# Kernel optimization log

Hardware: AMD Instinct MI355X
Metric: run time of the kernel (lower is better)

## Reference

```python
import jax, jax.numpy as jnp
import numpy as np

NUM_HEADS = 12
TOPK = 90


def setup_inputs() -> dict:
    key = jax.random.key(0)
    k1, k2, k3 = jax.random.split(key, 3)
    B, N, C = 8, 512, 768
    x = jax.random.normal(k1, (B, N, C), dtype=jnp.float32)
    qkv_w = jax.random.normal(k2, (3 * C, C), dtype=jnp.float32) * (C ** -0.5)
    proj_w = jax.random.normal(k3, (C, C), dtype=jnp.float32) * (C ** -0.5)
    proj_b = jnp.zeros((C,), dtype=jnp.float32)
    return {"x": x, "qkv_w": qkv_w, "proj_w": proj_w, "proj_b": proj_b, "islast": 0}


def reference(x, qkv_w, proj_w, proj_b, islast):
    B, N, C = x.shape
    H = NUM_HEADS
    hd = C // H
    scale = hd ** -0.5
    # qkv projection (no bias), split into q,k,v heads: [B,H,N,hd]
    qkv = (x @ qkv_w.T).reshape(B, N, 3, H, hd).transpose(2, 0, 3, 1, 4)
    q, k, v = qkv[0], qkv[1], qkv[2]
    attn = jnp.einsum('bhnd,bhmd->bhnm', q, k) * scale  # [B,H,N,N]
    if not islast:
        # keep only the top-k scores per row (kth-value threshold == topk mask)
        kth = jax.lax.top_k(attn, TOPK)[0][..., -1:]  # [B,H,N,1]
        attn = jnp.where(attn >= kth, attn, -jnp.inf)
    attn = jax.nn.softmax(attn, axis=-1)
    out = jnp.einsum('bhnm,bhmd->bnhd', attn, v).reshape(B, N, C)
    out = out @ proj_w.T + proj_b
    return out, attn
```

## Files before the change

kernel.cpp:

```cpp
#include <hip/hip_runtime.h>
#include <math.h>

#define BB 8
#define NN 512
#define CC 768
#define HH 12
#define HD 64
#define TOPK 90
#define QKV_ELEMS (BB*HH*NN*HD)
#define KC 2304

typedef __attribute__((ext_vector_type(8))) short short8;
typedef __attribute__((ext_vector_type(4))) float floatx4;

__device__ inline unsigned short f2bf(float f) {
    unsigned int u = __float_as_uint(f);
    u += 0x7FFFu + ((u >> 16) & 1u);
    return (unsigned short)(u >> 16);
}
__device__ inline float bf2f(unsigned short h) {
    return __uint_as_float(((unsigned int)h) << 16);
}

template<bool IS_A>
__global__ __launch_bounds__(256) void split_k(const float* __restrict__ in,
                                               unsigned short* __restrict__ o2,
                                               int total) {
    int idx = blockIdx.x * 256 + threadIdx.x;
    if (idx >= total) return;
    int e = idx * 4;
    int m = e / CC, kk = e - m * CC;
    float4 f = *(const float4*)(in + e);
    ushort4 hi, lo;
    hi.x = f2bf(f.x); lo.x = f2bf(f.x - bf2f(hi.x));
    hi.y = f2bf(f.y); lo.y = f2bf(f.y - bf2f(hi.y));
    hi.z = f2bf(f.z); lo.z = f2bf(f.z - bf2f(hi.z));
    hi.w = f2bf(f.w); lo.w = f2bf(f.w - bf2f(hi.w));
    unsigned short* base = o2 + (size_t)m * KC + kk;
    *(ushort4*)(base)        = hi;
    *(ushort4*)(base + CC)   = IS_A ? hi : lo;
    *(ushort4*)(base + 2*CC) = IS_A ? lo : hi;
}

template<int NCOLS, bool QKV_EPI>
__global__ __launch_bounds__(256) void gemm_split(const unsigned short* __restrict__ A,
                                                  const unsigned short* __restrict__ Bm,
                                                  const float* __restrict__ bias,
                                                  float* __restrict__ out,
                                                  unsigned short* __restrict__ qh,
                                                  unsigned short* __restrict__ ql,
                                                  unsigned short* __restrict__ kh,
                                                  unsigned short* __restrict__ kl,
                                                  unsigned short* __restrict__ vth,
                                                  unsigned short* __restrict__ vtl) {
    __shared__ char lds[32768];
    const int bm = blockIdx.x, bn = blockIdx.y;
    const int tid  = threadIdx.x;
    const int wave = tid >> 6, lane = tid & 63;
    const int wm = wave >> 1, wn = wave & 1;
    const int quad = lane >> 4, r = lane & 15;

    const unsigned short* gbase[8];
#pragma unroll
    for (int i = 0; i < 8; ++i) {
        int c = tid + i*256;
        int s = c & 1023;
        int m = s >> 3, octp = s & 7, oct = octp ^ (m & 7);
        gbase[i] = (i < 4 ? A  + (size_t)(bm*128 + m) * KC
                          : Bm + (size_t)(bn*128 + m) * KC) + oct*8;
    }

    int aoff[2][4], boff[2][4];
#pragma unroll
    for (int kb = 0; kb < 2; ++kb)
#pragma unroll
        for (int i = 0; i < 4; ++i) {
            int ra = wm*64 + i*16 + r;
            int rb2 = wn*64 + i*16 + r;
            aoff[kb][i] = (ra*8 + ((kb*4 + quad) ^ (ra & 7))) * 16;
            boff[kb][i] = 16384 + (rb2*8 + ((kb*4 + quad) ^ (rb2 & 7))) * 16;
        }

    floatx4 acc[4][4];
#pragma unroll
    for (int i = 0; i < 4; ++i)
#pragma unroll
        for (int j = 0; j < 4; ++j)
            acc[i][j] = (floatx4){0.f, 0.f, 0.f, 0.f};

    for (int it = 0; it < KC/64; ++it) {
        __syncthreads();
#pragma unroll
        for (int i = 0; i < 8; ++i) {
            __builtin_amdgcn_global_load_lds(
                (const __attribute__((address_space(1))) unsigned int*)gbase[i],
                (__attribute__((address_space(3))) unsigned int*)(lds + i*4096 + wave*1024),
                16, 0, 0);
            gbase[i] += 64;
        }
        asm volatile("s_waitcnt vmcnt(0)" ::: "memory");
        __syncthreads();

#pragma unroll
        for (int kb = 0; kb < 2; ++kb) {
            short8 af[4], bf[4];
#pragma unroll
            for (int i = 0; i < 4; ++i) af[i] = *(const short8*)(lds + aoff[kb][i]);
#pragma unroll
            for (int j = 0; j < 4; ++j) bf[j] = *(const short8*)(lds + boff[kb][j]);
#pragma unroll
            for (int i = 0; i < 4; ++i)
#pragma unroll
                for (int j = 0; j < 4; ++j)
                    acc[i][j] = __builtin_amdgcn_mfma_f32_16x16x32_bf16(af[i], bf[j], acc[i][j], 0, 0, 0);
        }
    }

    if (QKV_EPI) {
#pragma unroll
        for (int j = 0; j < 4; ++j) {
            int col = bn*128 + wn*64 + j*16 + r;
            int t = col / CC;
            int rem = col - t*CC;
            int h = rem >> 6, d = rem & 63;
            if (t == 2) {
#pragma unroll
                for (int i = 0; i < 4; ++i) {
                    int m0 = bm*128 + wm*64 + i*16 + quad*4;
                    int b = m0 >> 9, n0 = m0 & 511;
                    ushort4 hi, lo;
                    hi.x = f2bf(acc[i][j][0]); lo.x = f2bf(acc[i][j][0] - bf2f(hi.x));
                    hi.y = f2bf(acc[i][j][1]); lo.y = f2bf(acc[i][j][1] - bf2f(hi.y));
                    hi.z = f2bf(acc[i][j][2]); lo.z = f2bf(acc[i][j][2] - bf2f(hi.z));
                    hi.w = f2bf(acc[i][j][3]); lo.w = f2bf(acc[i][j][3] - bf2f(hi.w));
                    size_t off = ((size_t)((b*HH + h)*HD + d))*NN + n0;
                    *(ushort4*)(vth + off) = hi;
                    *(ushort4*)(vtl + off) = lo;
                }
            } else {
                unsigned short* ph = (t == 0) ? qh : kh;
                unsigned short* pl = (t == 0) ? ql : kl;
#pragma unroll
                for (int i = 0; i < 4; ++i) {
#pragma unroll
                    for (int e = 0; e < 4; ++e) {
                        int m = bm*128 + wm*64 + i*16 + quad*4 + e;
                        int b = m >> 9, nrow = m & 511;
                        size_t idx = ((size_t)(b*HH + h)*NN + nrow)*HD + d;
                        float val = acc[i][j][e];
                        unsigned short hi = f2bf(val);
                        ph[idx] = hi;
                        pl[idx] = f2bf(val - bf2f(hi));
                    }
                }
            }
        }
    } else {
#pragma unroll
        for (int j = 0; j < 4; ++j) {
            int col = bn*128 + wn*64 + j*16 + r;
            float bv = bias[col];
#pragma unroll
            for (int i = 0; i < 4; ++i) {
#pragma unroll
                for (int e = 0; e < 4; ++e) {
                    int m = bm*128 + wm*64 + i*16 + quad*4 + e;
                    out[(size_t)m*NCOLS + col] = acc[i][j][e] + bv;
                }
            }
        }
    }
}

__global__ __launch_bounds__(256, 1) void attn_scores_k(
        const unsigned short* __restrict__ qh, const unsigned short* __restrict__ ql,
        const unsigned short* __restrict__ kh, const unsigned short* __restrict__ kl,
        const unsigned short* __restrict__ vth, const unsigned short* __restrict__ vtl,
        const int* __restrict__ islast, float* __restrict__ attn,
        unsigned short* __restrict__ Ao) {

    __shared__ char smem[34816];
    unsigned short* qs = (unsigned short*)smem;
    char* ks = smem + 18432;

    const int bh = blockIdx.x % 96;
    const int rb = blockIdx.x / 96;
    const int tid = threadIdx.x;
    const int wv = tid >> 6, lane = tid & 63;
    const int quad = lane >> 4, r = lane & 15;
    const int b = bh / HH, h = bh % HH;

    const unsigned short* gq[2] = { qh + ((size_t)bh*NN + rb*64)*HD,
                                    ql + ((size_t)bh*NN + rb*64)*HD };
#pragma unroll
    for (int i = 0; i < 4; ++i) {
        int s = tid + i*256;
        int hl = s >> 9, s2 = s & 511;
        int row = s2 >> 3, oct = s2 & 7;
        short8 val = *(const short8*)(gq[hl] + row*HD + oct*8);
        *(short8*)&qs[(hl*64 + row)*72 + oct*8] = val;
    }
    __syncthreads();

    short8 afr[6];
    {
        const int arow = wv*16 + r;
#pragma unroll
        for (int t = 0; t < 3; ++t) {
            int src = (t == 2) ? 1 : 0;
#pragma unroll
            for (int half = 0; half < 2; ++half)
                afr[t*2+half] = *(const short8*)&qs[(src*64 + arow)*72 + half*32 + quad*8];
        }
    }

    floatx4 acc[32];
#pragma unroll
    for (int ct = 0; ct < 32; ++ct) acc[ct] = (floatx4){0.f,0.f,0.f,0.f};

    const unsigned short* gk[2] = { kh + (size_t)bh*NN*HD, kl + (size_t)bh*NN*HD };

    for (int ch = 0; ch < 8; ++ch) {
        __syncthreads();
#pragma unroll
        for (int i = 0; i < 4; ++i) {
            int s = tid + i*256;
            int hl = s >> 9, s2 = s & 511;
            int row = s2 >> 3, octp = s2 & 7;
            int oct = octp ^ (row & 7);
            const unsigned short* src = gk[hl] + (size_t)(ch*64 + row)*HD + oct*8;
            __builtin_amdgcn_global_load_lds(
                (const __attribute__((address_space(1))) unsigned int*)src,
                (__attribute__((address_space(3))) unsigned int*)(ks + (size_t)(i*256 + wv*64)*16),
                16, 0, 0);
        }
        asm volatile("s_waitcnt vmcnt(0)" ::: "memory");
        __syncthreads();

#pragma unroll
        for (int ctl = 0; ctl < 4; ++ctl) {
            const int ct = ch*4 + ctl;
            const int n = ctl*16 + r;
#pragma unroll
            for (int t = 0; t < 3; ++t) {
                const int srcB = (t == 1) ? 1 : 0;
#pragma unroll
                for (int half = 0; half < 2; ++half) {
                    const int oct = (half*4 + quad) ^ (n & 7);
                    short8 bfr = *(const short8*)(ks + srcB*8192 + n*128 + oct*16);
                    acc[ct] = __builtin_amdgcn_mfma_f32_16x16x32_bf16(afr[t*2+half], bfr, acc[ct], 0, 0, 0);
                }
            }
        }
    }

    const int lastv = islast[0];

#pragma unroll
    for (int e = 0; e < 4; ++e) {
        unsigned int key[32];
#pragma unroll
        for (int ct = 0; ct < 32; ++ct) {
            unsigned int t = __float_as_uint(acc[ct][e] * 0.125f);
            key[ct] = (t & 0x80000000u) ? ~t : (t | 0x80000000u);
        }

        unsigned int kth = 0u;
        if (!lastv) {
            unsigned int uo = key[0], ua = key[0];
#pragma unroll
            for (int ct = 1; ct < 32; ++ct) { uo |= key[ct]; ua &= key[ct]; }
#pragma unroll
            for (int off = 1; off <= 8; off <<= 1) {
                uo |= __shfl_xor(uo, off);
                ua &= __shfl_xor(ua, off);
            }
            unsigned int diff = uo ^ ua;
            int bit = 31 - __clz(diff);
            unsigned int am = 0xFFFFFFFFu;
            int kk = TOPK, cntA = 512;
            int done = (diff == 0u);
            while (__ballot(!done) != 0ull) {
                if (!done) {
                    unsigned int m1 = 0u;
#pragma unroll
                    for (int ct = 0; ct < 32; ++ct)
                        m1 |= ((key[ct] >> bit) & 1u) << ct;
                    int c1 = __popc(am & m1);
                    c1 += __shfl_xor(c1, 1);
                    c1 += __shfl_xor(c1, 2);
                    c1 += __shfl_xor(c1, 4);
                    c1 += __shfl_xor(c1, 8);
                    if (kk <= c1) { am &= m1; cntA = c1; }
                    else          { kk -= c1; am &= ~m1; cntA -= c1; }
                    --bit;
                    done = (cntA == kk) | (kk == 1) | (bit < 0);
                }
            }
            unsigned int mn = 0xFFFFFFFFu, mx = 0u;
#pragma unroll
            for (int ct = 0; ct < 32; ++ct) {
                if ((am >> ct) & 1u) {
                    mn = mn < key[ct] ? mn : key[ct];
                    mx = mx > key[ct] ? mx : key[ct];
                }
            }
#pragma unroll
            for (int off = 1; off <= 8; off <<= 1) {
                unsigned int mns = __shfl_xor(mn, off), mxs = __shfl_xor(mx, off);
                mn = mn < mns ? mn : mns; mx = mx > mxs ? mx : mxs;
            }
            kth = (kk == 1) ? mx : mn;
        }

        unsigned int umx = key[0];
#pragma unroll
        for (int ct = 1; ct < 32; ++ct) umx = umx > key[ct] ? umx : key[ct];
#pragma unroll
        for (int off = 1; off <= 8; off <<= 1) {
            unsigned int t2 = __shfl_xor(umx, off);
            umx = umx > t2 ? umx : t2;
        }
        float fmx = __uint_as_float((umx & 0x80000000u) ? (umx & 0x7FFFFFFFu) : ~umx);
        float sum = 0.f;
#pragma unroll
        for (int ct = 0; ct < 32; ++ct) {
            unsigned int uu = key[ct];
            float f = __uint_as_float((uu & 0x80000000u) ? (uu & 0x7FFFFFFFu) : ~uu);
            float ev = (lastv || uu >= kth) ? __expf(f - fmx) : 0.f;
            acc[ct][e] = ev;
            sum += ev;
        }
#pragma unroll
        for (int off = 1; off <= 8; off <<= 1) sum += __shfl_xor(sum, off);
        const float inv = 1.f / sum;
        float* arow = attn + ((size_t)bh*NN + rb*64 + wv*16 + quad*4 + e) * NN;
#pragma unroll
        for (int ct = 0; ct < 32; ++ct) {
            float p = acc[ct][e] * inv;
            acc[ct][e] = p;
            arow[ct*16 + r] = p;
        }
    }

    unsigned short* pls = (unsigned short*)smem;
    char* vhs = smem + 10240;
    char* vls = smem + 18432;
    const unsigned short* gvh = vth + (size_t)bh*HD*NN;
    const unsigned short* gvl = vtl + (size_t)bh*HD*NN;

    floatx4 accO[4];
#pragma unroll
    for (int j = 0; j < 4; ++j) accO[j] = (floatx4){0.f,0.f,0.f,0.f};

    for (int ch = 0; ch < 8; ++ch) {
        __syncthreads();
#pragma unroll
        for (int ctl = 0; ctl < 4; ++ctl) {
            int col = ctl*16 + r;
#pragma unroll
            for (int e = 0; e < 4; ++e)
                pls[(wv*16 + quad*4 + e)*80 + col] = f2bf(acc[ch*4 + ctl][e]);
        }
#pragma unroll
        for (int i = 0; i < 2; ++i) {
            int s = tid + i*256;
            int d = s >> 3, octp = s & 7, oct = octp ^ (d & 7);
            size_t goff = (size_t)d*NN + ch*64 + oct*8;
            __builtin_amdgcn_global_load_lds(
                (const __attribute__((address_space(1))) unsigned int*)(gvh + goff),
                (__attribute__((address_space(3))) unsigned int*)(vhs + (i*256 + wv*64)*16),
                16, 0, 0);
            __builtin_amdgcn_global_load_lds(
                (const __attribute__((address_space(1))) unsigned int*)(gvl + goff),
                (__attribute__((address_space(3))) unsigned int*)(vls + (i*256 + wv*64)*16),
                16, 0, 0);
        }
        asm volatile("s_waitcnt vmcnt(0)" ::: "memory");
        __syncthreads();

#pragma unroll
        for (int kb = 0; kb < 2; ++kb) {
            short8 af = *(const short8*)&pls[(wv*16 + r)*80 + kb*32 + quad*8];
#pragma unroll
            for (int j = 0; j < 4; ++j) {
                int d = j*16 + r;
                int oct = (kb*4 + quad) ^ (d & 7);
                short8 bh8 = *(const short8*)(vhs + d*128 + oct*16);
                short8 bl8 = *(const short8*)(vls + d*128 + oct*16);
                accO[j] = __builtin_amdgcn_mfma_f32_16x16x32_bf16(af, bh8, accO[j], 0, 0, 0);
                accO[j] = __builtin_amdgcn_mfma_f32_16x16x32_bf16(af, bl8, accO[j], 0, 0, 0);
            }
        }
    }

#pragma unroll
    for (int j = 0; j < 4; ++j) {
        int d = j*16 + r;
#pragma unroll
        for (int e = 0; e < 4; ++e) {
            int n = rb*64 + wv*16 + quad*4 + e;
            size_t mrow = (size_t)b*NN + n;
            float val = accO[j][e];
            unsigned short hi = f2bf(val);
            unsigned short lo = f2bf(val - bf2f(hi));
            unsigned short* base = Ao + mrow*KC + h*HD + d;
            base[0] = hi; base[CC] = hi; base[2*CC] = lo;
        }
    }
}

extern "C" void kernel_launch(void* const* d_in, const int* in_sizes, int n_in,
                              void* d_out, int out_size, void* d_ws, size_t ws_size,
                              hipStream_t stream) {
    const float* x      = (const float*)d_in[0];
    const float* qkv_w  = (const float*)d_in[1];
    const float* proj_w = (const float*)d_in[2];
    const float* proj_b = (const float*)d_in[3];
    const int*   islast = (const int*)d_in[4];

    float* out  = (float*)d_out;
    float* attn = out + (size_t)BB*NN*CC;

    unsigned short* us = (unsigned short*)d_ws;
    unsigned short* vth = us;
    unsigned short* vtl = vth + (size_t)QKV_ELEMS;
    unsigned short* qhp = vtl + (size_t)QKV_ELEMS;
    unsigned short* qlp = qhp + (size_t)QKV_ELEMS;
    unsigned short* khp = qlp + (size_t)QKV_ELEMS;
    unsigned short* klp = khp + (size_t)QKV_ELEMS;
    unsigned short* Asp   = klp + (size_t)QKV_ELEMS;
    unsigned short* Bqkv  = Asp  + (size_t)4096*KC;
    unsigned short* Bproj = Bqkv + (size_t)2304*KC;

    split_k<true> <<<dim3(4096*CC/4/256), 256, 0, stream>>>(x,      Asp,   4096*CC/4);
    split_k<false><<<dim3(2304*CC/4/256), 256, 0, stream>>>(qkv_w,  Bqkv,  2304*CC/4);
    split_k<false><<<dim3(CC*CC/4/256),   256, 0, stream>>>(proj_w, Bproj, CC*CC/4);

    gemm_split<0, true>  <<<dim3(32, 18), 256, 0, stream>>>(Asp, Bqkv, nullptr, nullptr,
                                                            qhp, qlp, khp, klp, vth, vtl);
    attn_scores_k        <<<dim3(96*8),   256, 0, stream>>>(qhp, qlp, khp, klp, vth, vtl,
                                                            islast, attn, Asp);
    gemm_split<CC, false><<<dim3(32, 6),  256, 0, stream>>>(Asp, Bproj, proj_b, out,
                                                            nullptr, nullptr, nullptr, nullptr,
                                                            nullptr, nullptr);
}
```

Baseline: 357.3 us.

## Double-buffer K and V LDS tiles to overlap global loads with MFMA

The score and PV loops in the attention kernel now ping-pong between two LDS buffers. The next chunk of K (and later V) is issued with global_load_lds before the MFMAs on the current chunk run, so load latency can hide behind compute. The first V chunk is prefetched during the last K iteration. One barrier per iteration is removed, at the cost of more shared memory (51 KB) and tighter reasoning about which LDS regions are live at each point.

```diff
diff --git a/kernel.cpp b/kernel.cpp
--- a/kernel.cpp
+++ b/kernel.cpp
@@ -179,9 +179,8 @@
         const int* __restrict__ islast, float* __restrict__ attn,
         unsigned short* __restrict__ Ao) {
 
-    __shared__ char smem[34816];
+    __shared__ char smem[51200];
     unsigned short* qs = (unsigned short*)smem;
-    char* ks = smem + 18432;
 
     const int bh = blockIdx.x % 96;
     const int rb = blockIdx.x / 96;
@@ -202,6 +201,23 @@
     }
     __syncthreads();
 
+    const unsigned short* gk[2] = { kh + (size_t)bh*NN*HD, kl + (size_t)bh*NN*HD };
+    const unsigned short* gvh = vth + (size_t)bh*HD*NN;
+    const unsigned short* gvl = vtl + (size_t)bh*HD*NN;
+
+#pragma unroll
+    for (int i = 0; i < 4; ++i) {
+        int s = tid + i*256;
+        int hl = s >> 9, s2 = s & 511;
+        int row = s2 >> 3, octp = s2 & 7;
+        int oct = octp ^ (row & 7);
+        const unsigned short* src = gk[hl] + (size_t)row*HD + oct*8;
+        __builtin_amdgcn_global_load_lds(
+            (const __attribute__((address_space(1))) unsigned int*)src,
+            (__attribute__((address_space(3))) unsigned int*)(smem + 18432 + (size_t)(i*256 + wv*64)*16),
+            16, 0, 0);
+    }
+
     short8 afr[6];
     {
         const int arow = wv*16 + r;
@@ -218,24 +234,40 @@
 #pragma unroll
     for (int ct = 0; ct < 32; ++ct) acc[ct] = (floatx4){0.f,0.f,0.f,0.f};
 
-    const unsigned short* gk[2] = { kh + (size_t)bh*NN*HD, kl + (size_t)bh*NN*HD };
-
     for (int ch = 0; ch < 8; ++ch) {
-        __syncthreads();
-#pragma unroll
-        for (int i = 0; i < 4; ++i) {
-            int s = tid + i*256;
-            int hl = s >> 9, s2 = s & 511;
-            int row = s2 >> 3, octp = s2 & 7;
-            int oct = octp ^ (row & 7);
-            const unsigned short* src = gk[hl] + (size_t)(ch*64 + row)*HD + oct*8;
-            __builtin_amdgcn_global_load_lds(
-                (const __attribute__((address_space(1))) unsigned int*)src,
-                (__attribute__((address_space(3))) unsigned int*)(ks + (size_t)(i*256 + wv*64)*16),
-                16, 0, 0);
-        }
+        char* kcur = smem + 18432 + (ch & 1)*16384;
         asm volatile("s_waitcnt vmcnt(0)" ::: "memory");
         __syncthreads();
+        if (ch < 7) {
+            char* knxt = smem + 18432 + ((ch + 1) & 1)*16384;
+#pragma unroll
+            for (int i = 0; i < 4; ++i) {
+                int s = tid + i*256;
+                int hl = s >> 9, s2 = s & 511;
+                int row = s2 >> 3, octp = s2 & 7;
+                int oct = octp ^ (row & 7);
+                const unsigned short* src = gk[hl] + (size_t)((ch + 1)*64 + row)*HD + oct*8;
+                __builtin_amdgcn_global_load_lds(
+                    (const __attribute__((address_space(1))) unsigned int*)src,
+                    (__attribute__((address_space(3))) unsigned int*)(knxt + (size_t)(i*256 + wv*64)*16),
+                    16, 0, 0);
+            }
+        } else {
+#pragma unroll
+            for (int i = 0; i < 2; ++i) {
+                int s = tid + i*256;
+                int d = s >> 3, octp = s & 7, oct = octp ^ (d & 7);
+                size_t goff = (size_t)d*NN + oct*8;
+                __builtin_amdgcn_global_load_lds(
+                    (const __attribute__((address_space(1))) unsigned int*)(gvh + goff),
+                    (__attribute__((address_space(3))) unsigned int*)(smem + 10240 + (i*256 + wv*64)*16),
+                    16, 0, 0);
+                __builtin_amdgcn_global_load_lds(
+                    (const __attribute__((address_space(1))) unsigned int*)(gvl + goff),
+                    (__attribute__((address_space(3))) unsigned int*)(smem + 18432 + (i*256 + wv*64)*16),
+                    16, 0, 0);
+            }
+        }
 
 #pragma unroll
         for (int ctl = 0; ctl < 4; ++ctl) {
@@ -247,7 +279,7 @@
 #pragma unroll
                 for (int half = 0; half < 2; ++half) {
                     const int oct = (half*4 + quad) ^ (n & 7);
-                    short8 bfr = *(const short8*)(ks + srcB*8192 + n*128 + oct*16);
+                    short8 bfr = *(const short8*)(kcur + srcB*8192 + n*128 + oct*16);
                     acc[ct] = __builtin_amdgcn_mfma_f32_16x16x32_bf16(afr[t*2+half], bfr, acc[ct], 0, 0, 0);
                 }
             }
@@ -344,17 +376,14 @@
     }
 
     unsigned short* pls = (unsigned short*)smem;
-    char* vhs = smem + 10240;
-    char* vls = smem + 18432;
-    const unsigned short* gvh = vth + (size_t)bh*HD*NN;
-    const unsigned short* gvl = vtl + (size_t)bh*HD*NN;
 
     floatx4 accO[4];
 #pragma unroll
     for (int j = 0; j < 4; ++j) accO[j] = (floatx4){0.f,0.f,0.f,0.f};
 
     for (int ch = 0; ch < 8; ++ch) {
-        __syncthreads();
+        char* vhs = smem + 10240 + (ch & 1)*16384;
+        char* vls = vhs + 8192;
 #pragma unroll
         for (int ctl = 0; ctl < 4; ++ctl) {
             int col = ctl*16 + r;
@@ -362,22 +391,26 @@
             for (int e = 0; e < 4; ++e)
                 pls[(wv*16 + quad*4 + e)*80 + col] = f2bf(acc[ch*4 + ctl][e]);
         }
-#pragma unroll
-        for (int i = 0; i < 2; ++i) {
-            int s = tid + i*256;
-            int d = s >> 3, octp = s & 7, oct = octp ^ (d & 7);
-            size_t goff = (size_t)d*NN + ch*64 + oct*8;
-            __builtin_amdgcn_global_load_lds(
-                (const __attribute__((address_space(1))) unsigned int*)(gvh + goff),
-                (__attribute__((address_space(3))) unsigned int*)(vhs + (i*256 + wv*64)*16),
-                16, 0, 0);
-            __builtin_amdgcn_global_load_lds(
-                (const __attribute__((address_space(1))) unsigned int*)(gvl + goff),
-                (__attribute__((address_space(3))) unsigned int*)(vls + (i*256 + wv*64)*16),
-                16, 0, 0);
-        }
         asm volatile("s_waitcnt vmcnt(0)" ::: "memory");
         __syncthreads();
+        if (ch < 7) {
+            char* nvh = smem + 10240 + ((ch + 1) & 1)*16384;
+            char* nvl = nvh + 8192;
+#pragma unroll
+            for (int i = 0; i < 2; ++i) {
+                int s = tid + i*256;
+                int d = s >> 3, octp = s & 7, oct = octp ^ (d & 7);
+                size_t goff = (size_t)d*NN + (ch + 1)*64 + oct*8;
+                __builtin_amdgcn_global_load_lds(
+                    (const __attribute__((address_space(1))) unsigned int*)(gvh + goff),
+                    (__attribute__((address_space(3))) unsigned int*)(nvh + (i*256 + wv*64)*16),
+                    16, 0, 0);
+                __builtin_amdgcn_global_load_lds(
+                    (const __attribute__((address_space(1))) unsigned int*)(gvl + goff),
+                    (__attribute__((address_space(3))) unsigned int*)(nvl + (i*256 + wv*64)*16),
+                    16, 0, 0);
+            }
+        }
 
 #pragma unroll
         for (int kb = 0; kb < 2; ++kb) {
```

Result: slower. 384.7 us (+7.7%).
